# Performance work log

Measured on AMD Instinct MI355X. Metric: run time of the kernel, lower is better.

Reference implementation:

```python
import jax, jax.numpy as jnp
import numpy as np

N_EMBED = 1024
EMBED_DIM = 256

def setup_inputs() -> dict:
    key = jax.random.key(0)
    k1, k2 = jax.random.split(key)
    hidden_states = jax.random.normal(k1, (64, 32, 32, EMBED_DIM), dtype=jnp.float32)
    emb_weights = jax.random.normal(k2, (N_EMBED, EMBED_DIM), dtype=jnp.float32)
    return {"hidden_states": hidden_states, "emb_weights": emb_weights}

def reference(hidden_states, emb_weights):
    # flatten (B,H,W,C) -> (N, C) with C == embed_dim
    z_flat = hidden_states.reshape((-1, EMBED_DIM))
    # squared distance: ||z||^2 + ||e||^2 - 2 z.e
    distance = (
        jnp.sum(z_flat ** 2, axis=1, keepdims=True)
        + jnp.sum(emb_weights ** 2, axis=1)
        - 2.0 * jnp.dot(z_flat, emb_weights.T)
    )  # (N, n_embed)
    min_encoding_indices = jnp.argmin(distance, axis=1)  # (N,)
    z_q = jnp.take(emb_weights, min_encoding_indices, axis=0).reshape(hidden_states.shape)
    min_encoding_indices = min_encoding_indices.reshape(hidden_states.shape[0], -1)
    return z_q, min_encoding_indices
```

## Files before the change

kernel.cpp:

```cpp
#include <hip/hip_runtime.h>

typedef _Float16 half8  __attribute__((ext_vector_type(8)));
typedef _Float16 half4  __attribute__((ext_vector_type(4)));
typedef float    float4v __attribute__((ext_vector_type(4)));

#define N_ROWS  65536
#define N_CODES 1024
#define DIM     256

__global__ __launch_bounds__(64)
void vq_prep(const float* __restrict__ emb, float* __restrict__ e_norm,
             _Float16* __restrict__ e_frag) {
    const int c = blockIdx.x, lane = threadIdx.x;
    const int l15 = c & 15, nt = c >> 4;
    float4v v = ((const float4v*)(emb + (size_t)c * DIM))[lane];
    half4 h, l;
    float ss = 0.f;
    #pragma unroll
    for (int j = 0; j < 4; ++j) {
        float x = v[j];
        ss += x * x;
        _Float16 hh = (_Float16)x;
        h[j] = hh;
        l[j] = (_Float16)(x - (float)hh);
    }
    const int ks = lane >> 3, q = (lane >> 1) & 3, jb = (lane & 1) * 4;
    _Float16* p = e_frag + ((size_t)(nt * 8 + ks)) * 1024 + (q * 16 + l15) * 8 + jb;
    *(half4*)p = h;
    *(half4*)(p + 512) = l;
    #pragma unroll
    for (int m = 32; m >= 1; m >>= 1) ss += __shfl_xor(ss, m, 64);
    if (lane == 0) e_norm[c] = ss;
}

__global__ __launch_bounds__(512, 2)
void vq_main(const float* __restrict__ z,
             const _Float16* __restrict__ e_frag,
             const float* __restrict__ e_norm,
             float2* __restrict__ partial) {
    __shared__ alignas(16) _Float16 sB[65536];

    const int t = threadIdx.x;
    const int w = t >> 6, lane = t & 63, quad = lane >> 4, l15 = lane & 15;
    const int bx = blockIdx.x;
    const int cg = (bx >> 3) & 3;
    const int rb = (bx & 7) | ((bx >> 5) << 3);
    const int rowbase = rb * 512 + w * 64;

    float bs[4][4];
    int   bi[4][4];
    #pragma unroll
    for (int mt = 0; mt < 4; ++mt)
        #pragma unroll
        for (int r = 0; r < 4; ++r) { bs[mt][r] = 3.4e38f; bi[mt][r] = 0; }

    for (int p = 0; p < 2; ++p) {
        if (p) __syncthreads();
        {
            const _Float16* gsrc = e_frag + (size_t)(16 * cg + 8 * p) * 8192;
            #pragma unroll
            for (int rr = 0; rr < 16; ++rr) {
                const int off = rr * 4096 + t * 8;
                *(half8*)(sB + off) = *(const half8*)(gsrc + off);
            }
        }
        __syncthreads();

        float nrm[8];
        #pragma unroll
        for (int ntl = 0; ntl < 8; ++ntl)
            nrm[ntl] = e_norm[cg * 256 + p * 128 + ntl * 16 + l15];

        float4v acc[4][8] = {};

        for (int ks = 0; ks < 8; ++ks) {
            half8 ah[4], al[4];
            #pragma unroll
            for (int mt = 0; mt < 4; ++mt) {
                const float* ap = z + (size_t)(rowbase + mt * 16 + l15) * DIM
                                    + ks * 32 + quad * 8;
                float4v a0 = *(const float4v*)ap;
                float4v a1 = *(const float4v*)(ap + 4);
                #pragma unroll
                for (int j = 0; j < 4; ++j) {
                    { float x = a0[j]; _Float16 hh = (_Float16)x;
                      ah[mt][j] = hh; al[mt][j] = (_Float16)(x - (float)hh); }
                    { float x = a1[j]; _Float16 hh = (_Float16)x;
                      ah[mt][4 + j] = hh; al[mt][4 + j] = (_Float16)(x - (float)hh); }
                }
            }
            #pragma unroll
            for (int ntl = 0; ntl < 8; ++ntl) {
                const _Float16* bp = sB + (ntl * 8 + ks) * 1024 + lane * 8;
                half8 bh = *(const half8*)bp;
                half8 bl = *(const half8*)(bp + 512);
                #pragma unroll
                for (int mt = 0; mt < 4; ++mt) {
                    acc[mt][ntl] = __builtin_amdgcn_mfma_f32_16x16x32_f16(ah[mt], bh, acc[mt][ntl], 0, 0, 0);
                    acc[mt][ntl] = __builtin_amdgcn_mfma_f32_16x16x32_f16(ah[mt], bl, acc[mt][ntl], 0, 0, 0);
                    acc[mt][ntl] = __builtin_amdgcn_mfma_f32_16x16x32_f16(al[mt], bh, acc[mt][ntl], 0, 0, 0);
                }
            }
        }

        #pragma unroll
        for (int mt = 0; mt < 4; ++mt)
            #pragma unroll
            for (int ntl = 0; ntl < 8; ++ntl) {
                const int code = cg * 256 + p * 128 + ntl * 16 + l15;
                #pragma unroll
                for (int r = 0; r < 4; ++r) {
                    float s = nrm[ntl] - 2.0f * acc[mt][ntl][r];
                    if (s < bs[mt][r]) { bs[mt][r] = s; bi[mt][r] = code; }
                }
            }
    }

    #pragma unroll
    for (int m = 1; m < 16; m <<= 1)
        #pragma unroll
        for (int mt = 0; mt < 4; ++mt)
            #pragma unroll
            for (int r = 0; r < 4; ++r) {
                float s2 = __shfl_xor(bs[mt][r], m, 64);
                int   i2 = __shfl_xor(bi[mt][r], m, 64);
                if (s2 < bs[mt][r] || (s2 == bs[mt][r] && i2 < bi[mt][r])) {
                    bs[mt][r] = s2; bi[mt][r] = i2;
                }
            }

    if (l15 == 0) {
        #pragma unroll
        for (int mt = 0; mt < 4; ++mt)
            #pragma unroll
            for (int r = 0; r < 4; ++r) {
                const int row = rowbase + mt * 16 + quad * 4 + r;
                float2 pr; pr.x = bs[mt][r]; pr.y = (float)bi[mt][r];
                partial[(size_t)row * 4 + cg] = pr;
            }
    }
}

__global__ __launch_bounds__(256)
void vq_reduce(const float2* __restrict__ partial, float* __restrict__ idxf) {
    const int r = blockIdx.x * 256 + threadIdx.x;
    const float2* p = partial + (size_t)r * 4;
    float bsv = p[0].x, biv = p[0].y;
    #pragma unroll
    for (int s = 1; s < 4; ++s) {
        float2 v = p[s];
        if (v.x < bsv || (v.x == bsv && v.y < biv)) { bsv = v.x; biv = v.y; }
    }
    idxf[r] = biv;
}

__global__ __launch_bounds__(256)
void vq_gather(const float* __restrict__ emb,
               const float* __restrict__ idxf,
               float* __restrict__ zq) {
    const int tid  = blockIdx.x * 256 + threadIdx.x;
    const int r    = tid >> 6;
    const int lane = tid & 63;
    const int idx  = (int)idxf[r];
    const float4* ep = (const float4*)(emb + (size_t)idx * DIM);
    ((float4*)(zq + (size_t)r * DIM))[lane] = ep[lane];
}

extern "C" void kernel_launch(void* const* d_in, const int* in_sizes, int n_in,
                              void* d_out, int out_size, void* d_ws, size_t ws_size,
                              hipStream_t stream) {
    const float* z   = (const float*)d_in[0];
    const float* emb = (const float*)d_in[1];

    float* zq   = (float*)d_out;
    float* idxf = zq + (size_t)N_ROWS * DIM;

    const size_t need = 4096 + (size_t)N_CODES * DIM * 2 * sizeof(_Float16)
                      + (size_t)N_ROWS * 4 * sizeof(float2);
    char* base = (ws_size >= need) ? (char*)d_ws : (char*)d_out;
    float*    e_norm  = (float*)base;
    _Float16* e_frag  = (_Float16*)(base + 4096);
    float2*   partial = (float2*)(e_frag + (size_t)N_CODES * DIM * 2);

    vq_prep<<<N_CODES, 64, 0, stream>>>(emb, e_norm, e_frag);
    vq_main<<<512, 512, 0, stream>>>(z, e_frag, e_norm, partial);
    vq_reduce<<<N_ROWS / 256, 256, 0, stream>>>(partial, idxf);
    vq_gather<<<(N_ROWS * 64) / 256, 256, 0, stream>>>(emb, idxf, zq);
}
```

Baseline: 238.4 us.

## Pre-split z into fp16 hi/lo fragments and shrink codebook tiles to 64 codes

Adds a prep kernel that converts z once into MFMA-ready fp16 hi/lo fragments, so the main kernel no longer repeats the fp32-to-fp16 split for every code group. The main kernel now uses a 128x16 grid with 64 codes per block, 32 KB of LDS and a higher occupancy target, and the row-wise reduction reads 16 partials per row. In exchange, the z fragments are re-read 16 times from global memory or cache, there is an extra kernel and a larger partial buffer, and a fallback path keeps inline conversion when workspace is small.

```diff
diff --git a/kernel.cpp b/kernel.cpp
--- a/kernel.cpp
+++ b/kernel.cpp
@@ -7,6 +7,10 @@
 #define N_ROWS  65536
 #define N_CODES 1024
 #define DIM     256
+#define CG          16
+#define CODES_PER_CG 64
+#define RB          128
+#define ROWS_PER_RB 512
 
 __global__ __launch_bounds__(64)
 void vq_prep(const float* __restrict__ emb, float* __restrict__ e_norm,
@@ -33,121 +37,206 @@
     if (lane == 0) e_norm[c] = ss;
 }
 
-__global__ __launch_bounds__(512, 2)
-void vq_main(const float* __restrict__ z,
-             const _Float16* __restrict__ e_frag,
-             const float* __restrict__ e_norm,
-             float2* __restrict__ partial) {
-    __shared__ alignas(16) _Float16 sB[65536];
+__global__ __launch_bounds__(64)
+void vq_prep_z(const float* __restrict__ z, _Float16* __restrict__ z_frag) {
+    const int mt = blockIdx.x;
+    const int lane = threadIdx.x, quad = lane >> 4, l15 = lane & 15;
+    const float* rowp = z + (size_t)(mt * 16 + l15) * DIM;
+    #pragma unroll
+    for (int ks = 0; ks < 8; ++ks) {
+        const float* p = rowp + ks * 32 + quad * 8;
+        float4v a0 = *(const float4v*)p;
+        float4v a1 = *(const float4v*)(p + 4);
+        half8 h, l;
+        #pragma unroll
+        for (int j = 0; j < 4; ++j) {
+            float x = a0[j]; _Float16 hx = (_Float16)x;
+            h[j] = hx; l[j] = (_Float16)(x - (float)hx);
+            float y = a1[j]; _Float16 hy = (_Float16)y;
+            h[4 + j] = hy; l[4 + j] = (_Float16)(y - (float)hy);
+        }
+        _Float16* dst = z_frag + ((size_t)mt * 8 + ks) * 1024 + lane * 8;
+        *(half8*)dst = h;
+        *(half8*)(dst + 512) = l;
+    }
+}
+
+__global__ __launch_bounds__(512, 4)
+void vq_main_pre(const _Float16* __restrict__ z_frag,
+                 const _Float16* __restrict__ e_frag,
+                 const float* __restrict__ e_norm,
+                 float2* __restrict__ partial) {
+    __shared__ _Float16 sB[32768];
+    __shared__ float s_nrm[CODES_PER_CG];
 
     const int t = threadIdx.x;
     const int w = t >> 6, lane = t & 63, quad = lane >> 4, l15 = lane & 15;
-    const int bx = blockIdx.x;
-    const int cg = (bx >> 3) & 3;
-    const int rb = (bx & 7) | ((bx >> 5) << 3);
-    const int rowbase = rb * 512 + w * 64;
-
-    float bs[4][4];
-    int   bi[4][4];
-    #pragma unroll
-    for (int mt = 0; mt < 4; ++mt)
-        #pragma unroll
-        for (int r = 0; r < 4; ++r) { bs[mt][r] = 3.4e38f; bi[mt][r] = 0; }
-
-    for (int p = 0; p < 2; ++p) {
-        if (p) __syncthreads();
-        {
-            const _Float16* gsrc = e_frag + (size_t)(16 * cg + 8 * p) * 8192;
-            #pragma unroll
-            for (int rr = 0; rr < 16; ++rr) {
-                const int off = rr * 4096 + t * 8;
-                *(half8*)(sB + off) = *(const half8*)(gsrc + off);
-            }
-        }
-        __syncthreads();
-
-        float nrm[8];
-        #pragma unroll
-        for (int ntl = 0; ntl < 8; ++ntl)
-            nrm[ntl] = e_norm[cg * 256 + p * 128 + ntl * 16 + l15];
-
-        float4v acc[4][8] = {};
-
-        for (int ks = 0; ks < 8; ++ks) {
-            half8 ah[4], al[4];
-            #pragma unroll
-            for (int mt = 0; mt < 4; ++mt) {
-                const float* ap = z + (size_t)(rowbase + mt * 16 + l15) * DIM
-                                    + ks * 32 + quad * 8;
-                float4v a0 = *(const float4v*)ap;
-                float4v a1 = *(const float4v*)(ap + 4);
-                #pragma unroll
-                for (int j = 0; j < 4; ++j) {
-                    { float x = a0[j]; _Float16 hh = (_Float16)x;
-                      ah[mt][j] = hh; al[mt][j] = (_Float16)(x - (float)hh); }
-                    { float x = a1[j]; _Float16 hh = (_Float16)x;
-                      ah[mt][4 + j] = hh; al[mt][4 + j] = (_Float16)(x - (float)hh); }
-                }
-            }
-            #pragma unroll
-            for (int ntl = 0; ntl < 8; ++ntl) {
-                const _Float16* bp = sB + (ntl * 8 + ks) * 1024 + lane * 8;
-                half8 bh = *(const half8*)bp;
-                half8 bl = *(const half8*)(bp + 512);
-                #pragma unroll
-                for (int mt = 0; mt < 4; ++mt) {
-                    acc[mt][ntl] = __builtin_amdgcn_mfma_f32_16x16x32_f16(ah[mt], bh, acc[mt][ntl], 0, 0, 0);
-                    acc[mt][ntl] = __builtin_amdgcn_mfma_f32_16x16x32_f16(ah[mt], bl, acc[mt][ntl], 0, 0, 0);
-                    acc[mt][ntl] = __builtin_amdgcn_mfma_f32_16x16x32_f16(al[mt], bh, acc[mt][ntl], 0, 0, 0);
-                }
-            }
-        }
-
-        #pragma unroll
-        for (int mt = 0; mt < 4; ++mt)
-            #pragma unroll
-            for (int ntl = 0; ntl < 8; ++ntl) {
-                const int code = cg * 256 + p * 128 + ntl * 16 + l15;
-                #pragma unroll
-                for (int r = 0; r < 4; ++r) {
-                    float s = nrm[ntl] - 2.0f * acc[mt][ntl][r];
-                    if (s < bs[mt][r]) { bs[mt][r] = s; bi[mt][r] = code; }
-                }
-            }
-    }
-
-    #pragma unroll
-    for (int m = 1; m < 16; m <<= 1)
-        #pragma unroll
-        for (int mt = 0; mt < 4; ++mt)
-            #pragma unroll
-            for (int r = 0; r < 4; ++r) {
-                float s2 = __shfl_xor(bs[mt][r], m, 64);
-                int   i2 = __shfl_xor(bi[mt][r], m, 64);
-                if (s2 < bs[mt][r] || (s2 == bs[mt][r] && i2 < bi[mt][r])) {
-                    bs[mt][r] = s2; bi[mt][r] = i2;
-                }
-            }
-
-    if (l15 == 0) {
-        #pragma unroll
-        for (int mt = 0; mt < 4; ++mt)
-            #pragma unroll
-            for (int r = 0; r < 4; ++r) {
+    const int rb = blockIdx.x, cg = blockIdx.y;
+
+    {
+        const _Float16* src = e_frag + (size_t)cg * 32768;
+        #pragma unroll
+        for (int i = 0; i < 8; ++i)
+            *(half8*)(sB + i * 4096 + t * 8) = *(const half8*)(src + i * 4096 + t * 8);
+        if (t < CODES_PER_CG) s_nrm[t] = e_norm[cg * CODES_PER_CG + t];
+    }
+    __syncthreads();
+
+    const int rt0 = rb * 32 + w * 4;
+    const int rowbase = rb * ROWS_PER_RB + w * 64;
+
+    float4v acc[4][4] = {};
+
+    for (int ks = 0; ks < 8; ++ks) {
+        half8 ah[4], al[4];
+        #pragma unroll
+        for (int mt = 0; mt < 4; ++mt) {
+            const _Float16* ap = z_frag + ((size_t)(rt0 + mt) * 8 + ks) * 1024 + lane * 8;
+            ah[mt] = *(const half8*)ap;
+            al[mt] = *(const half8*)(ap + 512);
+        }
+        #pragma unroll
+        for (int ntl = 0; ntl < 4; ++ntl) {
+            const _Float16* bp = sB + (ntl * 8 + ks) * 1024 + lane * 8;
+            half8 bh = *(const half8*)bp;
+            half8 bl = *(const half8*)(bp + 512);
+            #pragma unroll
+            for (int mt = 0; mt < 4; ++mt)
+                acc[mt][ntl] = __builtin_amdgcn_mfma_f32_16x16x32_f16(ah[mt], bh, acc[mt][ntl], 0, 0, 0);
+            #pragma unroll
+            for (int mt = 0; mt < 4; ++mt)
+                acc[mt][ntl] = __builtin_amdgcn_mfma_f32_16x16x32_f16(ah[mt], bl, acc[mt][ntl], 0, 0, 0);
+            #pragma unroll
+            for (int mt = 0; mt < 4; ++mt)
+                acc[mt][ntl] = __builtin_amdgcn_mfma_f32_16x16x32_f16(al[mt], bh, acc[mt][ntl], 0, 0, 0);
+        }
+    }
+
+    float nrm[4]; int cbase[4];
+    #pragma unroll
+    for (int ntl = 0; ntl < 4; ++ntl) {
+        cbase[ntl] = cg * CODES_PER_CG + ntl * 16 + l15;
+        nrm[ntl]   = s_nrm[ntl * 16 + l15];
+    }
+    #pragma unroll
+    for (int mt = 0; mt < 4; ++mt) {
+        #pragma unroll
+        for (int r = 0; r < 4; ++r) {
+            float bs = 0.f; int bi = 0;
+            #pragma unroll
+            for (int ntl = 0; ntl < 4; ++ntl) {
+                float s = nrm[ntl] - 2.0f * acc[mt][ntl][r];
+                if (ntl == 0 || s < bs) { bs = s; bi = cbase[ntl]; }
+            }
+            #pragma unroll
+            for (int m = 1; m < 16; m <<= 1) {
+                float s2 = __shfl_xor(bs, m, 64);
+                int   i2 = __shfl_xor(bi, m, 64);
+                if (s2 < bs || (s2 == bs && i2 < bi)) { bs = s2; bi = i2; }
+            }
+            if (l15 == 0) {
                 const int row = rowbase + mt * 16 + quad * 4 + r;
-                float2 pr; pr.x = bs[mt][r]; pr.y = (float)bi[mt][r];
-                partial[(size_t)row * 4 + cg] = pr;
-            }
+                float2 pr; pr.x = bs; pr.y = (float)bi;
+                partial[(size_t)row * CG + cg] = pr;
+            }
+        }
+    }
+}
+
+__global__ __launch_bounds__(512, 2)
+void vq_main_inl(const float* __restrict__ z,
+                 const _Float16* __restrict__ e_frag,
+                 const float* __restrict__ e_norm,
+                 float2* __restrict__ partial) {
+    __shared__ _Float16 sB[32768];
+    __shared__ float s_nrm[CODES_PER_CG];
+
+    const int t = threadIdx.x;
+    const int w = t >> 6, lane = t & 63, quad = lane >> 4, l15 = lane & 15;
+    const int rb = blockIdx.x, cg = blockIdx.y;
+
+    {
+        const _Float16* src = e_frag + (size_t)cg * 32768;
+        #pragma unroll
+        for (int i = 0; i < 8; ++i)
+            *(half8*)(sB + i * 4096 + t * 8) = *(const half8*)(src + i * 4096 + t * 8);
+        if (t < CODES_PER_CG) s_nrm[t] = e_norm[cg * CODES_PER_CG + t];
+    }
+    __syncthreads();
+
+    const int rowbase = rb * ROWS_PER_RB + w * 64;
+    float4v acc[4][4] = {};
+
+    for (int ks = 0; ks < 8; ++ks) {
+        half8 ah[4], al[4];
+        #pragma unroll
+        for (int mt = 0; mt < 4; ++mt) {
+            const float* ap = z + (size_t)(rowbase + mt * 16 + l15) * DIM + ks * 32 + quad * 8;
+            float4v a0 = *(const float4v*)ap;
+            float4v a1 = *(const float4v*)(ap + 4);
+            #pragma unroll
+            for (int j = 0; j < 4; ++j) {
+                float x = a0[j]; _Float16 hx = (_Float16)x;
+                ah[mt][j] = hx; al[mt][j] = (_Float16)(x - (float)hx);
+                float y = a1[j]; _Float16 hy = (_Float16)y;
+                ah[mt][4 + j] = hy; al[mt][4 + j] = (_Float16)(y - (float)hy);
+            }
+        }
+        #pragma unroll
+        for (int ntl = 0; ntl < 4; ++ntl) {
+            const _Float16* bp = sB + (ntl * 8 + ks) * 1024 + lane * 8;
+            half8 bh = *(const half8*)bp;
+            half8 bl = *(const half8*)(bp + 512);
+            #pragma unroll
+            for (int mt = 0; mt < 4; ++mt)
+                acc[mt][ntl] = __builtin_amdgcn_mfma_f32_16x16x32_f16(ah[mt], bh, acc[mt][ntl], 0, 0, 0);
+            #pragma unroll
+            for (int mt = 0; mt < 4; ++mt)
+                acc[mt][ntl] = __builtin_amdgcn_mfma_f32_16x16x32_f16(ah[mt], bl, acc[mt][ntl], 0, 0, 0);
+            #pragma unroll
+            for (int mt = 0; mt < 4; ++mt)
+                acc[mt][ntl] = __builtin_amdgcn_mfma_f32_16x16x32_f16(al[mt], bh, acc[mt][ntl], 0, 0, 0);
+        }
+    }
+
+    float nrm[4]; int cbase[4];
+    #pragma unroll
+    for (int ntl = 0; ntl < 4; ++ntl) {
+        cbase[ntl] = cg * CODES_PER_CG + ntl * 16 + l15;
+        nrm[ntl]   = s_nrm[ntl * 16 + l15];
+    }
+    #pragma unroll
+    for (int mt = 0; mt < 4; ++mt) {
+        #pragma unroll
+        for (int r = 0; r < 4; ++r) {
+            float bs = 0.f; int bi = 0;
+            #pragma unroll
+            for (int ntl = 0; ntl < 4; ++ntl) {
+                float s = nrm[ntl] - 2.0f * acc[mt][ntl][r];
+                if (ntl == 0 || s < bs) { bs = s; bi = cbase[ntl]; }
+            }
+            #pragma unroll
+            for (int m = 1; m < 16; m <<= 1) {
+                float s2 = __shfl_xor(bs, m, 64);
+                int   i2 = __shfl_xor(bi, m, 64);
+                if (s2 < bs || (s2 == bs && i2 < bi)) { bs = s2; bi = i2; }
+            }
+            if (l15 == 0) {
+                const int row = rowbase + mt * 16 + quad * 4 + r;
+                float2 pr; pr.x = bs; pr.y = (float)bi;
+                partial[(size_t)row * CG + cg] = pr;
+            }
+        }
     }
 }
 
 __global__ __launch_bounds__(256)
 void vq_reduce(const float2* __restrict__ partial, float* __restrict__ idxf) {
     const int r = blockIdx.x * 256 + threadIdx.x;
-    const float2* p = partial + (size_t)r * 4;
+    const float2* p = partial + (size_t)r * CG;
     float bsv = p[0].x, biv = p[0].y;
     #pragma unroll
-    for (int s = 1; s < 4; ++s) {
+    for (int s = 1; s < CG; ++s) {
         float2 v = p[s];
         if (v.x < bsv || (v.x == bsv && v.y < biv)) { bsv = v.x; biv = v.y; }
     }
@@ -175,15 +264,37 @@
     float* zq   = (float*)d_out;
     float* idxf = zq + (size_t)N_ROWS * DIM;
 
-    const size_t need = 4096 + (size_t)N_CODES * DIM * 2 * sizeof(_Float16)
-                      + (size_t)N_ROWS * 4 * sizeof(float2);
-    char* base = (ws_size >= need) ? (char*)d_ws : (char*)d_out;
-    float*    e_norm  = (float*)base;
-    _Float16* e_frag  = (_Float16*)(base + 4096);
-    float2*   partial = (float2*)(e_frag + (size_t)N_CODES * DIM * 2);
+    const size_t zfrag_b = (size_t)N_ROWS * DIM * 2 * sizeof(_Float16);
+    const size_t efrag_b = (size_t)N_CODES * DIM * 2 * sizeof(_Float16);
+    const size_t part_b  = (size_t)N_ROWS * CG * sizeof(float2);
+    const size_t small_b = 4096 + efrag_b + part_b;
+
+    char* small;
+    _Float16* z_frag = nullptr;
+    int pre;
+    if (ws_size >= zfrag_b + small_b) {
+        z_frag = (_Float16*)d_ws;
+        small  = (char*)d_ws + zfrag_b;
+        pre = 1;
+    } else if (ws_size >= small_b) {
+        z_frag = (_Float16*)zq;
+        small  = (char*)d_ws;
+        pre = 1;
+    } else {
+        small = (char*)zq;
+        pre = 0;
+    }
+    float*    e_norm  = (float*)small;
+    _Float16* e_frag  = (_Float16*)(small + 4096);
+    float2*   partial = (float2*)(small + 4096 + efrag_b);
 
     vq_prep<<<N_CODES, 64, 0, stream>>>(emb, e_norm, e_frag);
-    vq_main<<<512, 512, 0, stream>>>(z, e_frag, e_norm, partial);
+    if (pre) {
+        vq_prep_z<<<N_ROWS / 16, 64, 0, stream>>>(z, z_frag);
+        vq_main_pre<<<dim3(RB, CG), 512, 0, stream>>>(z_frag, e_frag, e_norm, partial);
+    } else {
+        vq_main_inl<<<dim3(RB, CG), 512, 0, stream>>>(z, e_frag, e_norm, partial);
+    }
     vq_reduce<<<N_ROWS / 256, 256, 0, stream>>>(partial, idxf);
     vq_gather<<<(N_ROWS * 64) / 256, 256, 0, stream>>>(emb, idxf, zq);
 }
```

After: 284.4 us. 19.3% more time.

## Restructure VQ main kernel: stage rows in LDS, stream codebook, fuse reduce and gather

Applied to the files above, without the earlier changes.

The main kernel now gives each block 64 rows, converts them once to split-fp16 hi/lo fragments in LDS, and has each of the 8 waves cover a distinct 128-code slice, reading codebook fragments directly from global/L2. This replaces the old 4-way codebook split with partial results. A block-level argmin in LDS produces the final index, and when workspace is available the gather of z_q is fused into the same kernel, removing the separate reduce and gather launches. The trade is that the codebook is re-read from L2 by every block instead of from LDS, and occupancy is requested at 4 blocks per CU.

```diff
diff --git a/kernel.cpp b/kernel.cpp
--- a/kernel.cpp
+++ b/kernel.cpp
@@ -7,6 +7,8 @@
 #define N_ROWS  65536
 #define N_CODES 1024
 #define DIM     256
+#define BM      64
+#define NB      (N_ROWS / BM)
 
 __global__ __launch_bounds__(64)
 void vq_prep(const float* __restrict__ emb, float* __restrict__ e_norm,
@@ -33,19 +35,49 @@
     if (lane == 0) e_norm[c] = ss;
 }
 
-__global__ __launch_bounds__(512, 2)
+__global__ __launch_bounds__(512, 4)
 void vq_main(const float* __restrict__ z,
              const _Float16* __restrict__ e_frag,
              const float* __restrict__ e_norm,
-             float2* __restrict__ partial) {
-    __shared__ alignas(16) _Float16 sB[65536];
+             const float* __restrict__ emb,
+             float* __restrict__ zq,
+             float* __restrict__ idxf,
+             int fused) {
+    __shared__ alignas(16) _Float16 sA[BM * DIM * 2];
+    __shared__ float  s_nrm[N_CODES];
+    __shared__ float2 s_best[BM][8];
+    __shared__ int    s_idx[BM];
 
     const int t = threadIdx.x;
     const int w = t >> 6, lane = t & 63, quad = lane >> 4, l15 = lane & 15;
-    const int bx = blockIdx.x;
-    const int cg = (bx >> 3) & 3;
-    const int rb = (bx & 7) | ((bx >> 5) << 3);
-    const int rowbase = rb * 512 + w * 64;
+    const int rowbase = blockIdx.x * BM;
+
+    s_nrm[t] = e_norm[t];
+    s_nrm[t + 512] = e_norm[t + 512];
+
+    {
+        const int row = t >> 3, ks = t & 7;
+        const int mt = row >> 4, l15r = row & 15;
+        const float4v* src = (const float4v*)(z + ((size_t)(rowbase + row)) * DIM + ks * 32);
+        float4v v[8];
+        #pragma unroll
+        for (int i = 0; i < 8; ++i) v[i] = src[i];
+        _Float16* dst = sA + (size_t)(mt * 8 + ks) * 1024 + l15r * 8;
+        #pragma unroll
+        for (int q = 0; q < 4; ++q) {
+            half8 h, l;
+            #pragma unroll
+            for (int j = 0; j < 4; ++j) {
+                float x = v[2 * q][j];     _Float16 hx = (_Float16)x;
+                h[j] = hx;                 l[j] = (_Float16)(x - (float)hx);
+                float y = v[2 * q + 1][j]; _Float16 hy = (_Float16)y;
+                h[4 + j] = hy;             l[4 + j] = (_Float16)(y - (float)hy);
+            }
+            *(half8*)(dst + q * 128) = h;
+            *(half8*)(dst + q * 128 + 512) = l;
+        }
+    }
+    __syncthreads();
 
     float bs[4][4];
     int   bi[4][4];
@@ -54,66 +86,48 @@
         #pragma unroll
         for (int r = 0; r < 4; ++r) { bs[mt][r] = 3.4e38f; bi[mt][r] = 0; }
 
-    for (int p = 0; p < 2; ++p) {
-        if (p) __syncthreads();
-        {
-            const _Float16* gsrc = e_frag + (size_t)(16 * cg + 8 * p) * 8192;
-            #pragma unroll
-            for (int rr = 0; rr < 16; ++rr) {
-                const int off = rr * 4096 + t * 8;
-                *(half8*)(sB + off) = *(const half8*)(gsrc + off);
-            }
-        }
-        __syncthreads();
-
-        float nrm[8];
-        #pragma unroll
-        for (int ntl = 0; ntl < 8; ++ntl)
-            nrm[ntl] = e_norm[cg * 256 + p * 128 + ntl * 16 + l15];
-
-        float4v acc[4][8] = {};
-
+    for (int chunk = 0; chunk < 2; ++chunk) {
+        float4v acc[4][4] = {};
+
+        #pragma unroll
         for (int ks = 0; ks < 8; ++ks) {
             half8 ah[4], al[4];
             #pragma unroll
             for (int mt = 0; mt < 4; ++mt) {
-                const float* ap = z + (size_t)(rowbase + mt * 16 + l15) * DIM
-                                    + ks * 32 + quad * 8;
-                float4v a0 = *(const float4v*)ap;
-                float4v a1 = *(const float4v*)(ap + 4);
-                #pragma unroll
-                for (int j = 0; j < 4; ++j) {
-                    { float x = a0[j]; _Float16 hh = (_Float16)x;
-                      ah[mt][j] = hh; al[mt][j] = (_Float16)(x - (float)hh); }
-                    { float x = a1[j]; _Float16 hh = (_Float16)x;
-                      ah[mt][4 + j] = hh; al[mt][4 + j] = (_Float16)(x - (float)hh); }
-                }
-            }
-            #pragma unroll
-            for (int ntl = 0; ntl < 8; ++ntl) {
-                const _Float16* bp = sB + (ntl * 8 + ks) * 1024 + lane * 8;
+                const _Float16* ap = sA + (size_t)(mt * 8 + ks) * 1024 + lane * 8;
+                ah[mt] = *(const half8*)ap;
+                al[mt] = *(const half8*)(ap + 512);
+            }
+            #pragma unroll
+            for (int ntl = 0; ntl < 4; ++ntl) {
+                const int nt = w * 8 + chunk * 4 + ntl;
+                const _Float16* bp = e_frag + ((size_t)nt * 8 + ks) * 1024 + lane * 8;
                 half8 bh = *(const half8*)bp;
                 half8 bl = *(const half8*)(bp + 512);
                 #pragma unroll
-                for (int mt = 0; mt < 4; ++mt) {
+                for (int mt = 0; mt < 4; ++mt)
                     acc[mt][ntl] = __builtin_amdgcn_mfma_f32_16x16x32_f16(ah[mt], bh, acc[mt][ntl], 0, 0, 0);
+                #pragma unroll
+                for (int mt = 0; mt < 4; ++mt)
                     acc[mt][ntl] = __builtin_amdgcn_mfma_f32_16x16x32_f16(ah[mt], bl, acc[mt][ntl], 0, 0, 0);
+                #pragma unroll
+                for (int mt = 0; mt < 4; ++mt)
                     acc[mt][ntl] = __builtin_amdgcn_mfma_f32_16x16x32_f16(al[mt], bh, acc[mt][ntl], 0, 0, 0);
-                }
-            }
-        }
-
-        #pragma unroll
-        for (int mt = 0; mt < 4; ++mt)
-            #pragma unroll
-            for (int ntl = 0; ntl < 8; ++ntl) {
-                const int code = cg * 256 + p * 128 + ntl * 16 + l15;
+            }
+        }
+
+        #pragma unroll
+        for (int ntl = 0; ntl < 4; ++ntl) {
+            const int code = w * 128 + chunk * 64 + ntl * 16 + l15;
+            const float nrm = s_nrm[code];
+            #pragma unroll
+            for (int mt = 0; mt < 4; ++mt)
                 #pragma unroll
                 for (int r = 0; r < 4; ++r) {
-                    float s = nrm[ntl] - 2.0f * acc[mt][ntl][r];
+                    float s = nrm - 2.0f * acc[mt][ntl][r];
                     if (s < bs[mt][r]) { bs[mt][r] = s; bi[mt][r] = code; }
                 }
-            }
+        }
     }
 
     #pragma unroll
@@ -128,30 +142,41 @@
                     bs[mt][r] = s2; bi[mt][r] = i2;
                 }
             }
-
     if (l15 == 0) {
         #pragma unroll
         for (int mt = 0; mt < 4; ++mt)
             #pragma unroll
             for (int r = 0; r < 4; ++r) {
-                const int row = rowbase + mt * 16 + quad * 4 + r;
+                const int row = mt * 16 + quad * 4 + r;
                 float2 pr; pr.x = bs[mt][r]; pr.y = (float)bi[mt][r];
-                partial[(size_t)row * 4 + cg] = pr;
-            }
-    }
-}
-
-__global__ __launch_bounds__(256)
-void vq_reduce(const float2* __restrict__ partial, float* __restrict__ idxf) {
-    const int r = blockIdx.x * 256 + threadIdx.x;
-    const float2* p = partial + (size_t)r * 4;
-    float bsv = p[0].x, biv = p[0].y;
-    #pragma unroll
-    for (int s = 1; s < 4; ++s) {
-        float2 v = p[s];
-        if (v.x < bsv || (v.x == bsv && v.y < biv)) { bsv = v.x; biv = v.y; }
-    }
-    idxf[r] = biv;
+                s_best[row][w] = pr;
+            }
+    }
+    __syncthreads();
+
+    if (t < BM) {
+        float2 p0 = s_best[t][0];
+        float bsv = p0.x, biv = p0.y;
+        #pragma unroll
+        for (int s = 1; s < 8; ++s) {
+            float2 pv = s_best[t][s];
+            if (pv.x < bsv || (pv.x == bsv && pv.y < biv)) { bsv = pv.x; biv = pv.y; }
+        }
+        s_idx[t] = (int)biv;
+        idxf[rowbase + t] = biv;
+    }
+
+    if (!fused) return;
+    __syncthreads();
+
+    {
+        const int row = t >> 3, part = t & 7;
+        const int code = s_idx[row];
+        const float4* eb = (const float4*)(emb + (size_t)code * DIM);
+        float4* oq = (float4*)(zq + (size_t)(rowbase + row) * DIM);
+        #pragma unroll
+        for (int i = 0; i < 8; ++i) oq[part + i * 8] = eb[part + i * 8];
+    }
 }
 
 __global__ __launch_bounds__(256)
@@ -175,15 +200,16 @@
     float* zq   = (float*)d_out;
     float* idxf = zq + (size_t)N_ROWS * DIM;
 
-    const size_t need = 4096 + (size_t)N_CODES * DIM * 2 * sizeof(_Float16)
-                      + (size_t)N_ROWS * 4 * sizeof(float2);
-    char* base = (ws_size >= need) ? (char*)d_ws : (char*)d_out;
-    float*    e_norm  = (float*)base;
-    _Float16* e_frag  = (_Float16*)(base + 4096);
-    float2*   partial = (float2*)(e_frag + (size_t)N_CODES * DIM * 2);
+    const size_t efrag_b = (size_t)N_CODES * DIM * 2 * sizeof(_Float16);
+    const size_t need = 4096 + efrag_b;
+
+    char* base = (ws_size >= need) ? (char*)d_ws : (char*)zq;
+    const int fused = (ws_size >= need);
+    float*    e_norm = (float*)base;
+    _Float16* e_frag = (_Float16*)(base + 4096);
 
     vq_prep<<<N_CODES, 64, 0, stream>>>(emb, e_norm, e_frag);
-    vq_main<<<512, 512, 0, stream>>>(z, e_frag, e_norm, partial);
-    vq_reduce<<<N_ROWS / 256, 256, 0, stream>>>(partial, idxf);
-    vq_gather<<<(N_ROWS * 64) / 256, 256, 0, stream>>>(emb, idxf, zq);
-}
+    vq_main<<<NB, 512, 0, stream>>>(z, e_frag, e_norm, emb, zq, idxf, fused);
+    if (!fused)
+        vq_gather<<<(N_ROWS * 64) / 256, 256, 0, stream>>>(emb, idxf, zq);
+}
```

Result: slower. 615.0 us (+158.0%).
